# Kernel optimization log

Measured on AMD Instinct MI355X. Metric: run time of the kernel, lower is better.

Reference implementation:

```python
import jax, jax.numpy as jnp
import numpy as np

NUM_INST = 32
EPS = 1e-5


def _conv(x, w, b, stride=1, pad=0):
    y = jax.lax.conv_general_dilated(
        x, w, (stride, stride), ((pad, pad), (pad, pad)),
        dimension_numbers=('NCHW', 'OIHW', 'NCHW'))
    return y + b[None, :, None, None]


def _deconv(x, w, b):
    # torch ConvTranspose2d(k=3, s=2, p=1, output_padding=1); w is (Cin, Cout, 3, 3)
    wf = jnp.flip(w, (2, 3)).transpose(1, 0, 2, 3)  # -> OIHW
    y = jax.lax.conv_general_dilated(
        x, wf, (1, 1), ((1, 2), (1, 2)), lhs_dilation=(2, 2),
        dimension_numbers=('NCHW', 'OIHW', 'NCHW'))
    return y + b[None, :, None, None]


def _inorm(x):
    m = x.mean((2, 3), keepdims=True)
    v = x.var((2, 3), keepdims=True)  # biased, matches InstanceNorm2d
    return (x - m) * jax.lax.rsqrt(v + EPS)


def _rpad(x, p=3):
    return jnp.pad(x, ((0, 0), (0, 0), (p, p), (p, p)), mode='reflect')


def _backbone(input, w0, b0, w1, b1, w2, b2, w3, b3, w4, b4,
              w5, b5, w6, b6, w7, b7, w8, b8, w9, b9):
    x = jax.nn.relu(_inorm(_conv(_rpad(input), w0, b0)))          # [B,16,H,W]
    x = jax.nn.relu(_inorm(_conv(x, w1, b1, stride=2, pad=1)))    # [B,32,H/2,..]
    x = jax.nn.relu(_inorm(_conv(x, w2, b2, stride=2, pad=1)))    # [B,64,H/4,..]
    x = jax.nn.relu(_inorm(_conv(x, w3, b3, stride=2, pad=1)))    # [B,128,H/8,..]
    x = jax.nn.relu(_inorm(_conv(x, w4, b4, stride=2, pad=1)))    # [B,256,H/16,..]
    x = jax.nn.relu(_inorm(_deconv(x, w5, b5)))                   # [B,128,H/8,..]
    x = jax.nn.relu(_inorm(_deconv(x, w6, b6)))                   # [B,64,H/4,..]
    x = jax.nn.relu(_inorm(_deconv(x, w7, b7)))                   # [B,32,H/2,..]
    x = jax.nn.relu(_inorm(_deconv(x, w8, b8)))                   # [B,16,H,W]
    return jnp.tanh(_conv(_rpad(x), w9, b9))                      # [B,Cout,H,W]


def _segment_mean(outputs, inst):
    # outputs [B,C,H,W]; inst [B,1,H,W] int labels shared across the batch.
    B, C, H, W = outputs.shape
    seg = inst.reshape(-1)                                # [B*H*W]
    feats = outputs.transpose(0, 2, 3, 1).reshape(-1, C)  # [B*H*W, C]
    sums = jax.ops.segment_sum(feats, seg, num_segments=NUM_INST)
    counts = jax.ops.segment_sum(jnp.ones((feats.shape[0],), feats.dtype), seg,
                                 num_segments=NUM_INST)
    means = sums / jnp.maximum(counts, 1.0)[:, None]      # [NUM_INST, C]
    out = means[seg].reshape(B, H, W, C).transpose(0, 3, 1, 2)
    return out


def setup_inputs() -> dict:
    key = jax.random.key(0)
    ks = jax.random.split(key, 16)
    B, Cin, Cout, H, W = 4, 3, 3, 512, 512
    inp = {
        'input': jax.random.normal(ks[0], (B, Cin, H, W), jnp.float32),
        'inst': jax.random.randint(ks[1], (B, 1, H, W), 0, NUM_INST, jnp.int32),
    }
    std = 0.02
    # conv weights OIHW; deconv weights torch-style (Cin, Cout, kH, kW)
    shapes = [
        ('w0', (16, Cin, 7, 7)), ('w1', (32, 16, 3, 3)), ('w2', (64, 32, 3, 3)),
        ('w3', (128, 64, 3, 3)), ('w4', (256, 128, 3, 3)),
        ('w5', (256, 128, 3, 3)), ('w6', (128, 64, 3, 3)),
        ('w7', (64, 32, 3, 3)), ('w8', (32, 16, 3, 3)), ('w9', (Cout, 16, 7, 7)),
    ]
    bias_dims = [16, 32, 64, 128, 256, 128, 64, 32, 16, Cout]
    for i, (name, shp) in enumerate(shapes):
        inp[name] = std * jax.random.normal(ks[2 + i], shp, jnp.float32)
        inp['b%d' % i] = jnp.zeros((bias_dims[i],), jnp.float32)
    return inp


def reference(input, inst, w0, b0, w1, b1, w2, b2, w3, b3, w4, b4,
              w5, b5, w6, b6, w7, b7, w8, b8, w9, b9):
    outputs = _backbone(input, w0, b0, w1, b1, w2, b2, w3, b3, w4, b4,
                        w5, b5, w6, b6, w7, b7, w8, b8, w9, b9)
    return _segment_mean(outputs, inst)
```

## Files before the change

### kernel.cpp

```cpp
#include <hip/hip_runtime.h>
#include <math.h>

#define EPS_F 1e-5f

typedef __attribute__((ext_vector_type(8))) short short8;
typedef __attribute__((ext_vector_type(4))) float f32x4;
typedef __attribute__((ext_vector_type(8))) unsigned short ushort8;
typedef __attribute__((ext_vector_type(4))) unsigned short ushort4v;
typedef __attribute__((ext_vector_type(4))) int int4v;

__device__ __forceinline__ int reflect512(int v) {
    v = v < 0 ? -v : v;
    return v >= 512 ? 1022 - v : v;
}

__device__ __forceinline__ int xcd_swz(int L, int n) {
    return (L & 7) * (n >> 3) + (L >> 3);
}

__device__ __forceinline__ ushort f2bf(float f) {
    union { float f; unsigned u; } v; v.f = f;
    unsigned r = v.u + 0x7FFFu + ((v.u >> 16) & 1u);
    return (ushort)(r >> 16);
}
__device__ __forceinline__ float bf2f(ushort u) {
    union { unsigned u; float f; } v; v.u = (unsigned)u << 16;
    return v.f;
}

__device__ __forceinline__ unsigned cvt_pk_bf16(float lo, float hi) {
    unsigned r;
    asm("v_cvt_pk_bf16_f32 %0, %1, %2" : "=v"(r) : "v"(lo), "v"(hi));
    return r;
}

__device__ __forceinline__ float fast_tanh(float x) {
    float cx = fminf(fmaxf(x, -9.f), 9.f);
    float e  = __builtin_amdgcn_exp2f(cx * 2.8853900817779268f);
    return (e - 1.f) * __builtin_amdgcn_rcpf(e + 1.f);
}

template<int CIN, int COUT, bool DEC>
__device__ __forceinline__ void wp_mid(
    const float* __restrict__ w, ushort* __restrict__ dst, int i)
{
    constexpr int CIP = ((CIN + 31) / 32) * 32;
    int ci = i % CIP;
    int oc = (i / CIP) % COUT;
    int t  = i / (CIP * COUT);
    float x = 0.f;
    if (ci < CIN)
        x = DEC ? w[((size_t)ci * COUT + oc) * 9 + t]
                : w[((size_t)oc * CIN + ci) * 9 + t];
    dst[i] = f2bf(x);
}

__device__ __forceinline__ void wp_l1(
    const float* __restrict__ w, ushort* __restrict__ dst, int i)
{
    int k  = i & 31;
    int oc = (i >> 5) & 31;
    int c  = i >> 10;
    int tapsel = k >> 4, ci = k & 15;
    int t = 2 * c + tapsel;
    float x = (t < 9) ? w[((size_t)oc * 16 + ci) * 9 + t] : 0.f;
    dst[i] = f2bf(x);
}

template<bool L9>
__device__ __forceinline__ void wp_7(
    const float* __restrict__ w, ushort* __restrict__ dst, int i)
{
    int j   = i & 7;
    int oc  = (i >> 3) & 15;
    int kqe = (i >> 7) & 3;
    int cn  = i >> 9;
    float x = 0.f;
    if (L9) {
        int k = kqe * 8 + j;
        int tapsel = k >> 4, ci = k & 15;
        int ty = cn >> 2, q = cn & 3;
        int tx = 2 * q + tapsel;
        if (tx < 7 && oc < 3 && ty < 7)
            x = w[((size_t)oc * 16 + ci) * 49 + ty * 7 + tx];
    } else {
        int k = kqe * 8 + j;
        int dx = k >> 2, ci = k & 3;
        if (dx < 7 && ci < 3)
            x = w[((size_t)oc * 3 + ci) * 49 + cn * 7 + dx];
    }
    dst[i] = f2bf(x);
}

struct WprepArgs {
    const float* w[10];
    ushort* d[10];
};

__global__ __launch_bounds__(256) void wprep_all(WprepArgs a)
{
    int bi = blockIdx.x;
    int t  = threadIdx.x;
    if      (bi < 20)   wp_l1(a.w[1], a.d[1], (bi        ) * 256 + t);
    else if (bi < 92)   wp_mid<32,  64,  false>(a.w[2], a.d[2], (bi - 20   ) * 256 + t);
    else if (bi < 380)  wp_mid<64,  128, false>(a.w[3], a.d[3], (bi - 92   ) * 256 + t);
    else if (bi < 1532) wp_mid<128, 256, false>(a.w[4], a.d[4], (bi - 380  ) * 256 + t);
    else if (bi < 2684) wp_mid<256, 128, true >(a.w[5], a.d[5], (bi - 1532 ) * 256 + t);
    else if (bi < 2972) wp_mid<128, 64,  true >(a.w[6], a.d[6], (bi - 2684 ) * 256 + t);
    else if (bi < 3044) wp_mid<64,  32,  true >(a.w[7], a.d[7], (bi - 2972 ) * 256 + t);
    else if (bi < 3062) wp_mid<32,  16,  true >(a.w[8], a.d[8], (bi - 3044 ) * 256 + t);
    else if (bi < 3076) wp_7<false>(a.w[0], a.d[0], (bi - 3062) * 256 + t);
    else                wp_7<true >(a.w[9], a.d[9], (bi - 3076) * 256 + t);
}

template<int CIN, int COUT, int WIN, int MODE, int NWN, int MSUB, int RT, int CT>
__global__ __launch_bounds__(256) void mfconv(
    const ushort* __restrict__ in, const ushort* __restrict__ wbf,
    const float* __restrict__ bias, ushort* __restrict__ out,
    const float* __restrict__ stats_in, float invHWin,
    float* __restrict__ stats_out)
{
    constexpr int HWIN = WIN * WIN;
    constexpr int WOUT = (MODE == 0) ? (WIN / 2) : (WIN * 2);
    constexpr int HWOUT = WOUT * WOUT;
    constexpr int NMG = 4 / NWN;
    constexpr int NOC = NWN * 16;
    constexpr int M = NMG * MSUB * 16;
    static_assert(M == RT * CT, "tile mismatch");
    constexpr int SPAN = (MODE == 0) ? WOUT : WIN;
    constexpr int XC = SPAN / CT, YC = SPAN / RT;
    constexpr int NG = COUT / NOC;
    constexpr int NR = (MODE == 0) ? (2 * RT + 1) : (RT + 1);
    constexpr int NCO = (MODE == 0) ? (2 * CT + 1) : (CT + 1);
    constexpr int NPIX = NR * NCO;
    constexpr int CIP = ((CIN + 31) / 32) * 32;
    constexpr int NQ = (MODE == 0) ? 1 : 4;
    constexpr int LPW = 36;
    constexpr int NPOUT = (MODE == 0 ? 1 : 4) * M;
    constexpr int NOCP = NOC + 8;

    constexpr int TDY[9] = {1,1,1,0,0,0,0,0,0};
    constexpr int TDX[9] = {1,0,0,1,0,0,1,0,0};
    constexpr int TQ [9] = {3,2,3,1,0,1,3,2,3};

    extern __shared__ ushort sa[];
    __shared__ float mrall[CIP][2];
    __shared__ float sred[4][16][2];

    const int tid = threadIdx.x;
    const int lane = tid & 63, wv = tid >> 6;
    const int ln = lane & 15, kq = lane >> 4;
    const int wn = wv % NWN, wm = wv / NWN;
    const int grp = tid & 3;

    int bi = xcd_swz(blockIdx.x, gridDim.x);
    const int xc = bi % XC; bi /= XC;
    const int yc = bi % YC; bi /= YC;
    const int g  = bi % NG;
    const int b  = bi / NG;

    const int ocg = g * NOC + wn * 16 + ln;
    const float b0 = bias[ocg];
    f32x4 acc[NQ][MSUB];
    #pragma unroll
    for (int q = 0; q < NQ; q++)
        #pragma unroll
        for (int s = 0; s < MSUB; s++)
            acc[q][s] = (f32x4){b0, b0, b0, b0};

    for (int e = tid; e < CIP; e += 256) {
        float m = 0.f, r = 0.f;
        if (e < CIN) {
            int c = b * CIN + e;
            float s1 = stats_in[2 * c], s2 = stats_in[2 * c + 1];
            m = s1 * invHWin;
            r = rsqrtf(fmaf(s2, invHWin, -m * m) + EPS_F);
        }
        mrall[e][0] = m; mrall[e][1] = r;
    }

    const ushort* inb = in + (size_t)b * HWIN * CIN;

    for (int c0 = 0; c0 < CIP; c0 += 32) {
        __syncthreads();
        const int ch0 = c0 + 8 * grp;
        float m8[8], r8[8];
        #pragma unroll
        for (int j = 0; j < 8; j++) { m8[j] = mrall[ch0 + j][0]; r8[j] = mrall[ch0 + j][1]; }
        for (int pix = tid >> 2; pix < NPIX; pix += 64) {
            int pr = pix / NCO, pc = pix - pr * NCO;
            int gy, gx;
            if (MODE == 0) { gy = 2 * (yc * RT) - 1 + pr; gx = 2 * (xc * CT) - 1 + pc; }
            else           { gy = yc * RT + pr;           gx = xc * CT + pc; }
            ushort8 pk;
            #pragma unroll
            for (int j = 0; j < 8; j++) pk[j] = 0;
            if ((unsigned)gy < (unsigned)WIN && (unsigned)gx < (unsigned)WIN && ch0 < CIN) {
                ushort8 raw = *(const ushort8*)(inb + (size_t)(gy * WIN + gx) * CIN + ch0);
                #pragma unroll
                for (int j = 0; j < 8; j++) {
                    float x = bf2f(raw[j]);
                    pk[j] = f2bf(fmaxf((x - m8[j]) * r8[j], 0.f));
                }
            }
            *(ushort8*)&sa[pix * LPW + grp * 8] = pk;
        }
        __syncthreads();
        #pragma unroll
        for (int t = 0; t < 9; t++) {
            short8 bfr = *(const short8*)&wbf[((size_t)t * COUT + ocg) * CIP + c0 + kq * 8];
            #pragma unroll
            for (int s = 0; s < MSUB; s++) {
                const int mb = wm * MSUB * 16 + s * 16;
                const int r = mb / CT, cb = mb % CT;
                int pix;
                if (MODE == 0) pix = (t / 3 + 2 * r) * NCO + 2 * (cb + ln) + t % 3;
                else           pix = (TDY[t] + r) * NCO + cb + ln + TDX[t];
                short8 afr = *(const short8*)&sa[pix * LPW + kq * 8];
                int qd = (MODE == 0) ? 0 : TQ[t];
                acc[qd][s] = __builtin_amdgcn_mfma_f32_16x16x32_bf16(afr, bfr, acc[qd][s], 0, 0, 0);
            }
        }
    }

    float s1 = 0.f, s2 = 0.f;
    #pragma unroll
    for (int q = 0; q < NQ; q++)
        #pragma unroll
        for (int s = 0; s < MSUB; s++)
            #pragma unroll
            for (int rg = 0; rg < 4; rg++) {
                float v = acc[q][s][rg];
                s1 += v; s2 = fmaf(v, v, s2);
            }
    s1 += __shfl_xor(s1, 16); s2 += __shfl_xor(s2, 16);
    s1 += __shfl_xor(s1, 32); s2 += __shfl_xor(s2, 32);
    if (lane < 16) { sred[wv][lane][0] = s1; sred[wv][lane][1] = s2; }

    __syncthreads();
    const int ocl = wn * 16 + ln;
    if (MODE == 0) {
        #pragma unroll
        for (int s = 0; s < MSUB; s++)
            #pragma unroll
            for (int rg = 0; rg < 4; rg++) {
                const int m = wm * MSUB * 16 + s * 16 + kq * 4 + rg;
                sa[m * NOCP + ocl] = f2bf(acc[0][s][rg]);
            }
    } else {
        #pragma unroll
        for (int q = 0; q < 4; q++) {
            const int dy = q >> 1, dx = q & 1;
            #pragma unroll
            for (int s = 0; s < MSUB; s++)
                #pragma unroll
                for (int rg = 0; rg < 4; rg++) {
                    const int m = wm * MSUB * 16 + s * 16 + kq * 4 + rg;
                    const int r = m / CT, c = m % CT;
                    const int lp = (2 * r + dy) * (2 * CT) + 2 * c + dx;
                    sa[lp * NOCP + ocl] = f2bf(acc[q][s][rg]);
                }
        }
    }
    __syncthreads();

    ushort* ob = out + (size_t)b * HWOUT * COUT + g * NOC;
    for (int e = tid; e < (NPOUT * NOC) / 8; e += 256) {
        int u = e * 8;
        int lp = u / NOC, co = u % NOC;
        int gp;
        if (MODE == 0) {
            int r = lp / CT, c = lp % CT;
            gp = (yc * RT + r) * WOUT + xc * CT + c;
        } else {
            int r2 = lp / (2 * CT), x2 = lp % (2 * CT);
            gp = (2 * (yc * RT) + r2) * WOUT + 2 * (xc * CT) + x2;
        }
        *(ushort8*)&ob[(size_t)gp * COUT + co] = *(const ushort8*)&sa[lp * NOCP + co];
    }

    if (tid < NOC) {
        int wnn = tid >> 4, oc = tid & 15;
        float t1 = 0.f, t2 = 0.f;
        #pragma unroll
        for (int k = 0; k < NMG; k++) {
            t1 += sred[wnn + k * NWN][oc][0];
            t2 += sred[wnn + k * NWN][oc][1];
        }
        int cix = b * COUT + g * NOC + wnn * 16 + oc;
        atomicAdd(&stats_out[2 * cix],     t1);
        atomicAdd(&stats_out[2 * cix + 1], t2);
    }
}

__global__ __launch_bounds__(256) void mfconv_l1(
    const ushort* __restrict__ in, const ushort* __restrict__ wbf,
    const float* __restrict__ bias, ushort* __restrict__ out,
    const float* __restrict__ stats_in, float invHWin,
    float* __restrict__ stats_out)
{
    constexpr int WIN = 512, HWIN = WIN * WIN;
    constexpr int WOUT = 256, HWOUT = WOUT * WOUT;
    constexpr int COUT = 32, RT = 4, CT = 32;
    constexpr int NCO = 65, NPIX = 585;
    constexpr int NOCP = 40;

    extern __shared__ ushort sa[];
    __shared__ float mrall[16][2];
    __shared__ float sred[4][16][2];

    const int tid = threadIdx.x;
    const int lane = tid & 63, wv = tid >> 6;
    const int ln = lane & 15, kq = lane >> 4;
    const int wn = wv & 1, wm = wv >> 1;

    int bi = xcd_swz(blockIdx.x, gridDim.x);
    const int xc = bi & 7;
    const int yc = (bi >> 3) & 63;
    const int b  = bi >> 9;

    const int ocg = wn * 16 + ln;
    const float b0 = bias[ocg];
    f32x4 acc[4];
    #pragma unroll
    for (int s = 0; s < 4; s++) acc[s] = (f32x4){b0, b0, b0, b0};

    if (tid < 16) {
        int c = b * 16 + tid;
        float s1 = stats_in[2 * c], s2 = stats_in[2 * c + 1];
        float m = s1 * invHWin;
        mrall[tid][0] = m;
        mrall[tid][1] = rsqrtf(fmaf(s2, invHWin, -m * m) + EPS_F);
    }

    const int grp = tid & 1, p0 = tid >> 1;
    const ushort* inb = in + (size_t)b * HWIN * 16 + grp * 8;
    ushort8 rw[5];
    bool ok[5];
    #pragma unroll
    for (int i = 0; i < 5; i++) {
        int pix = p0 + i * 128;
        int pr = pix / NCO, pc = pix - pr * NCO;
        int gy = 2 * (yc * RT) - 1 + pr;
        int gx = 2 * (xc * CT) - 1 + pc;
        ok[i] = (pix < NPIX) && ((unsigned)gy < (unsigned)WIN)
                             && ((unsigned)gx < (unsigned)WIN);
        if (ok[i])
            rw[i] = *(const ushort8*)(inb + (size_t)(gy * WIN + gx) * 16);
    }
    __syncthreads();

    float m8[8], r8[8];
    #pragma unroll
    for (int j = 0; j < 8; j++) {
        m8[j] = mrall[grp * 8 + j][0];
        r8[j] = mrall[grp * 8 + j][1];
    }
    #pragma unroll
    for (int i = 0; i < 5; i++) {
        int pix = p0 + i * 128;
        if (pix < NPIX) {
            ushort8 pk;
            #pragma unroll
            for (int j = 0; j < 8; j++) pk[j] = 0;
            if (ok[i]) {
                #pragma unroll
                for (int j = 0; j < 8; j++) {
                    float x = bf2f(rw[i][j]);
                    pk[j] = f2bf(fmaxf((x - m8[j]) * r8[j], 0.f));
                }
            }
            int ep = (pix * 16 + grp * 8) ^ (((pix >> 2) & 1) << 3);
            *(ushort8*)&sa[ep] = pk;
        }
    }
    __syncthreads();

    const int tp = kq >> 1, off8 = (kq & 1) * 8;
    #pragma unroll
    for (int c = 0; c < 5; c++) {
        short8 bfr = *(const short8*)&wbf[(size_t)(c * COUT + ocg) * 32 + kq * 8];
        int t = 2 * c + tp; t = t > 8 ? 8 : t;
        const int ty = t / 3, tx = t - 3 * ty;
        #pragma unroll
        for (int s = 0; s < 4; s++) {
            const int mb = wm * 64 + s * 16;
            const int r = mb >> 5, cb = mb & 31;
            int px = (ty + 2 * r) * NCO + 2 * (cb + ln) + tx;
            int ep = (px * 16 + off8) ^ (((px >> 2) & 1) << 3);
            short8 afr = *(const short8*)&sa[ep];
            acc[s] = __builtin_amdgcn_mfma_f32_16x16x32_bf16(afr, bfr, acc[s], 0, 0, 0);
        }
    }

    float s1 = 0.f, s2 = 0.f;
    #pragma unroll
    for (int s = 0; s < 4; s++)
        #pragma unroll
        for (int rg = 0; rg < 4; rg++) {
            float v = acc[s][rg];
            s1 += v; s2 = fmaf(v, v, s2);
        }
    s1 += __shfl_xor(s1, 16); s2 += __shfl_xor(s2, 16);
    s1 += __shfl_xor(s1, 32); s2 += __shfl_xor(s2, 32);
    if (lane < 16) { sred[wv][lane][0] = s1; sred[wv][lane][1] = s2; }

    __syncthreads();
    const int ocl = wn * 16 + ln;
    #pragma unroll
    for (int s = 0; s < 4; s++)
        #pragma unroll
        for (int rg = 0; rg < 4; rg++) {
            const int m = wm * 64 + s * 16 + kq * 4 + rg;
            sa[m * NOCP + ocl] = f2bf(acc[s][rg]);
        }
    __syncthreads();
    ushort* ob = out + (size_t)b * HWOUT * COUT;
    for (int e = tid; e < 512; e += 256) {
        int u = e * 8;
        int lp = u >> 5, co = u & 31;
        int r = lp >> 5, c = lp & 31;
        int gp = (yc * RT + r) * WOUT + xc * CT + c;
        *(ushort8*)&ob[(size_t)gp * COUT + co] = *(const ushort8*)&sa[lp * NOCP + co];
    }
    if (tid < 32) {
        int wnn = tid >> 4, oc = tid & 15;
        float t1 = 0.f, t2 = 0.f;
        #pragma unroll
        for (int k = 0; k < 2; k++) {
            t1 += sred[wnn + k * 2][oc][0];
            t2 += sred[wnn + k * 2][oc][1];
        }
        int cix = b * COUT + wnn * 16 + oc;
        atomicAdd(&stats_out[2 * cix],     t1);
        atomicAdd(&stats_out[2 * cix + 1], t2);
    }
}

template<bool BFIN, bool SEG>
__global__ __launch_bounds__(256, 4) void conv7x(
    const float* __restrict__ inf, const ushort* __restrict__ inb16,
    const ushort* __restrict__ wpk, const float* __restrict__ bias,
    ushort* __restrict__ out,
    const float* __restrict__ stats_in, float invHWin,
    float* __restrict__ stats_out,
    const int* __restrict__ inst, float* __restrict__ segacc)
{
    constexpr int W = 512, HW = 512 * 512;
    constexpr int TCOL = BFIN ? 32 : 64;
    constexpr int HCOL = TCOL + 6;
    constexpr int NPIXH = 14 * HCOL;
    constexpr int STR = BFIN ? 16 : 4;
    constexpr int SASZ = BFIN ? (532 * 16 + 32) : 12288;
    constexpr int XCN = 512 / TCOL;
    constexpr int NS = BFIN ? 4 : 8;

    __shared__ ushort sa[SASZ];
    __shared__ float mr[16][2];
    __shared__ float segl[SEG ? 128 : 1];
    __shared__ float sred[4][16][2];

    const int tid = threadIdx.x;
    const int lane = tid & 63, wv = tid >> 6;
    const int ln = lane & 15, kq = lane >> 4;

    int bi = xcd_swz(blockIdx.x, gridDim.x);
    const int xc = bi % XCN;
    const int yr = (bi / XCN) & 63;
    const int b  = bi / (XCN * 64);
    const int y0 = yr * 8, x0 = xc * TCOL;

    if constexpr (SEG) { if (tid < 128) segl[tid] = 0.f; }
    if constexpr (BFIN) {
        if (tid < 16) {
            int c = b * 16 + tid;
            float s1 = stats_in[2 * c], s2 = stats_in[2 * c + 1];
            float m = s1 * invHWin;
            mr[tid][0] = m;
            mr[tid][1] = rsqrtf(fmaf(s2, invHWin, -m * m) + EPS_F);
        }
        if (tid >= 32 && tid < 64) sa[532 * 16 + (tid - 32)] = 0;
        __syncthreads();
        const int h = tid & 1;
        float r8[8], nm8[8];
        #pragma unroll
        for (int j = 0; j < 8; j++) {
            r8[j]  = mr[8 * h + j][1];
            nm8[j] = -mr[8 * h + j][0] * r8[j];
        }
        const ushort* inb = inb16 + (size_t)b * HW * 16 + 8 * h;
        for (int pix = tid >> 1; pix < NPIXH; pix += 128) {
            int pr = pix / HCOL, pc = pix - pr * HCOL;
            int gy = reflect512(y0 - 3 + pr);
            int gx = reflect512(x0 - 3 + pc);
            ushort8 raw = *(const ushort8*)(inb + (size_t)(gy * W + gx) * 16);
            union { ushort8 us; unsigned u[4]; } P;
            #pragma unroll
            for (int q2 = 0; q2 < 4; q2++) {
                float lo = fmaxf(fmaf(bf2f(raw[2 * q2]),     r8[2 * q2],     nm8[2 * q2]),     0.f);
                float hi = fmaxf(fmaf(bf2f(raw[2 * q2 + 1]), r8[2 * q2 + 1], nm8[2 * q2 + 1]), 0.f);
                P.u[q2] = cvt_pk_bf16(lo, hi);
            }
            *(ushort8*)&sa[pix * STR + 8 * h] = P.us;
        }
    } else {
        const float* p0 = inf + (size_t)b * 3 * HW;
        for (int pix = tid; pix < NPIXH; pix += 256) {
            int pr = pix / HCOL, pc = pix - pr * HCOL;
            int gy = reflect512(y0 - 3 + pr);
            int gx = reflect512(x0 - 3 + pc);
            const float* p = p0 + gy * W + gx;
            ushort4v pk;
            pk[0] = f2bf(p[0]); pk[1] = f2bf(p[HW]);
            pk[2] = f2bf(p[2 * (size_t)HW]); pk[3] = 0;
            *(ushort4v*)&sa[pix * 4] = pk;
        }
        if (tid < 16) sa[980 * 4 + tid] = 0;
    }
    __syncthreads();

    const float b0 = (ln < (BFIN ? 3 : 16)) ? bias[ln] : 0.f;
    f32x4 acc[NS];
    #pragma unroll
    for (int s = 0; s < NS; s++) acc[s] = (f32x4){b0, b0, b0, b0};

    if constexpr (BFIN) {
        const int wr = wv >> 1, wc = wv & 1;
        const int abase = ((wr * 4) * HCOL + wc * 16 + ln + (kq >> 1)) * STR + (kq & 1) * 8;
        const ushort* wp9 = wpk + ((size_t)kq * 16 + ln) * 8;
        #pragma unroll
        for (int q = 0; q < 4; q++) {
            short8 bw[7];
            #pragma unroll
            for (int ty = 0; ty < 7; ty++)
                bw[ty] = *(const short8*)(wp9 + (size_t)(ty * 4 + q) * 512);
            #pragma unroll
            for (int rr = 0; rr < 10; rr++) {
                short8 afr = *(const short8*)&sa[abase + q * (2 * STR) + rr * (HCOL * STR)];
                #pragma unroll
                for (int ty = 0; ty < 7; ty++) {
                    const int s = rr - ty;
                    if (s >= 0 && s < 4)
                        acc[s] = __builtin_amdgcn_mfma_f32_16x16x32_bf16(afr, bw[ty], acc[s], 0, 0, 0);
                }
            }
        }
    } else {
        const int c0 = wv * 16;
        const int abase = (c0 + ln + 2 * kq) * 4;
        const ushort* wp0 = wpk + ((size_t)kq * 16 + ln) * 8;
        short8 bw[7];
        #pragma unroll
        for (int ty = 0; ty < 7; ty++)
            bw[ty] = *(const short8*)(wp0 + (size_t)ty * 512);
        #pragma unroll
        for (int R = 0; R < 14; R++) {
            short8 afr = *(const short8*)&sa[abase + R * (HCOL * 4)];
            #pragma unroll
            for (int ty = 0; ty < 7; ty++) {
                const int s = R - ty;
                if (s >= 0 && s < 8)
                    acc[s] = __builtin_amdgcn_mfma_f32_16x16x32_bf16(afr, bw[ty], acc[s], 0, 0, 0);
            }
        }
    }

    if constexpr (SEG) {
        const int wr = wv >> 1, wc = wv & 1;
        float* sf = (float*)sa;
        __syncthreads();
        if (ln < 3) {
            #pragma unroll
            for (int s = 0; s < 4; s++)
                #pragma unroll
                for (int rg = 0; rg < 4; rg++) {
                    int m = (wr * 4 + s) * 32 + wc * 16 + kq * 4 + rg;
                    sf[m * 5 + ln] = acc[s][rg];
                }
        }
        __syncthreads();
        const int* ib = inst + ((size_t)b << 18);
        {
            int p2 = tid;
            int r = p2 >> 5, c = p2 & 31;
            int lab = ib[(y0 + r) * W + x0 + c] & 31;
            atomicAdd(&segl[lab * 4 + 0], fast_tanh(sf[p2 * 5 + 0]));
            atomicAdd(&segl[lab * 4 + 1], fast_tanh(sf[p2 * 5 + 1]));
            atomicAdd(&segl[lab * 4 + 2], fast_tanh(sf[p2 * 5 + 2]));
            atomicAdd(&segl[lab * 4 + 3], 1.f);
        }
        __syncthreads();
        if (tid < 128) {
            float v = segl[tid];
            if (v != 0.f)
                atomicAdd(&segacc[(blockIdx.x & 7) * 128 + tid], v);
        }
    } else {
        float s1 = 0.f, s2 = 0.f;
        #pragma unroll
        for (int s = 0; s < NS; s++)
            #pragma unroll
            for (int rg = 0; rg < 4; rg++) {
                float v = acc[s][rg];
                s1 += v; s2 = fmaf(v, v, s2);
            }
        s1 += __shfl_xor(s1, 16); s2 += __shfl_xor(s2, 16);
        s1 += __shfl_xor(s1, 32); s2 += __shfl_xor(s2, 32);
        if (lane < 16) { sred[wv][lane][0] = s1; sred[wv][lane][1] = s2; }

        __syncthreads();
        #pragma unroll
        for (int s = 0; s < 8; s++)
            #pragma unroll
            for (int rg = 0; rg < 4; rg++) {
                int m = s * 64 + wv * 16 + kq * 4 + rg;
                sa[m * 24 + ln] = f2bf(acc[s][rg]);
            }
        __syncthreads();
        ushort* ob = out + (size_t)b * HW * 16;
        for (int e = tid; e < 1024; e += 256) {
            int u = e * 8;
            int lp = u >> 4, co = u & 15;
            int gp = (y0 + (lp >> 6)) * W + x0 + (lp & 63);
            *(ushort8*)&ob[(size_t)gp * 16 + co] = *(const ushort8*)&sa[lp * 24 + co];
        }
        if (tid < 16) {
            float t1 = 0.f, t2 = 0.f;
            #pragma unroll
            for (int k = 0; k < 4; k++) { t1 += sred[k][tid][0]; t2 += sred[k][tid][1]; }
            int cix = b * 16 + tid;
            atomicAdd(&stats_out[2 * cix],     t1);
            atomicAdd(&stats_out[2 * cix + 1], t2);
        }
    }
}

#define HW9 262144
__global__ void seg_final(const float* __restrict__ acc, float* __restrict__ means)
{
    int i = threadIdx.x;
    if (i < 96) {
        int s = i / 3, c = i - s * 3;
        float num = 0.f, den = 0.f;
        #pragma unroll
        for (int k = 0; k < 8; k++) {
            num += acc[k * 128 + s * 4 + c];
            den += acc[k * 128 + s * 4 + 3];
        }
        means[i] = num / fmaxf(den, 1.f);
    }
}

__global__ __launch_bounds__(256) void seg_scatter(
    const int* __restrict__ inst, const float* __restrict__ means,
    float* __restrict__ out)
{
    int p4 = blockIdx.x * 256 + threadIdx.x;
    int b  = p4 >> 16;
    int r4 = (p4 & 65535) * 4;
    const int4v labs = *(const int4v*)(inst + ((size_t)b << 18) + r4);
    float* ob = out + (size_t)b * 3 * HW9 + r4;
    f32x4 o0, o1, o2;
    #pragma unroll
    for (int j = 0; j < 4; j++) {
        int l3 = (labs[j] & 31) * 3;
        o0[j] = means[l3]; o1[j] = means[l3 + 1]; o2[j] = means[l3 + 2];
    }
    *(f32x4*)(ob)           = o0;
    *(f32x4*)(ob + HW9)     = o1;
    *(f32x4*)(ob + 2 * HW9) = o2;
}

extern "C" void kernel_launch(void* const* d_in, const int* in_sizes, int n_in,
                              void* d_out, int out_size, void* d_ws, size_t ws_size,
                              hipStream_t stream)
{
    const float* x_in = (const float*)d_in[0];
    const int*   inst = (const int*)d_in[1];
    const float* W_[10];
    const float* Bs[10];
    for (int i = 0; i < 10; i++) {
        W_[i] = (const float*)d_in[2 + 2 * i];
        Bs[i] = (const float*)d_in[3 + 2 * i];
    }
    float* out = (float*)d_out;

    ushort* Ab  = (ushort*)d_ws;
    ushort* Bb2 = Ab + (size_t)16777216;
    float*  st  = (float*)(Bb2 + (size_t)8388608);
    const int coff[9] = {0, 128, 384, 896, 1920, 3968, 4992, 5504, 5760};
    float* s_[9];
    for (int i = 0; i < 9; i++) s_[i] = st + coff[i];
    float* segacc = st + 5888;
    float* means  = st + 6912;
    ushort* wb = (ushort*)(st + 8192);
    const size_t OW1 = 0, OW2 = 9216, OW3 = 27648, OW4 = 101376,
                 OW5 = 396288, OW6 = 691200, OW7 = 764928, OW8 = 783360;
    ushort* wb0 = wb + 790000;
    ushort* wb9 = wb0 + 6656;

    hipMemsetAsync(st, 0, 6912 * sizeof(float), stream);

    WprepArgs wa;
    for (int i = 0; i < 10; i++) wa.w[i] = W_[i];
    wa.d[0] = wb0;
    wa.d[1] = wb + OW1; wa.d[2] = wb + OW2; wa.d[3] = wb + OW3; wa.d[4] = wb + OW4;
    wa.d[5] = wb + OW5; wa.d[6] = wb + OW6; wa.d[7] = wb + OW7; wa.d[8] = wb + OW8;
    wa.d[9] = wb9;
    wprep_all<<<dim3(3132), dim3(256), 0, stream>>>(wa);

    conv7x<false, false><<<dim3(2048), dim3(256), 0, stream>>>(
        x_in, nullptr, wb0, Bs[0], Ab, nullptr, 0.f, s_[0], nullptr, nullptr);

    mfconv_l1<<<dim3(2048), dim3(256), 18720, stream>>>(
        Ab, wb + OW1, Bs[1], Bb2, s_[0], 1.f / 262144.f, s_[1]);

    mfconv<32, 64, 256, 0, 2, 4, 4, 32><<<dim3(1024), dim3(256), 42120, stream>>>(
        Bb2, wb + OW2, Bs[2], Ab, s_[1], 1.f / 65536.f, s_[2]);

    mfconv<64, 128, 128, 0, 2, 4, 4, 32><<<dim3(512), dim3(256), 42120, stream>>>(
        Ab, wb + OW3, Bs[3], Bb2, s_[2], 1.f / 16384.f, s_[3]);

    mfconv<128, 256, 64, 0, 2, 2, 2, 32><<<dim3(512), dim3(256), 23400, stream>>>(
        Bb2, wb + OW4, Bs[4], Ab, s_[3], 1.f / 4096.f, s_[4]);

    mfconv<256, 128, 32, 1, 1, 1, 2, 32><<<dim3(512), dim3(256), 12288, stream>>>(
        Ab, wb + OW5, Bs[5], Bb2, s_[4], 1.f / 1024.f, s_[5]);

    mfconv<128, 64, 64, 1, 2, 2, 2, 32><<<dim3(512), dim3(256), 20480, stream>>>(
        Bb2, wb + OW6, Bs[6], Ab, s_[5], 1.f / 4096.f, s_[6]);

    mfconv<64, 32, 128, 1, 2, 2, 2, 32><<<dim3(1024), dim3(256), 20480, stream>>>(
        Ab, wb + OW7, Bs[7], Bb2, s_[6], 1.f / 16384.f, s_[7]);

    mfconv<32, 16, 256, 1, 1, 2, 2, 64><<<dim3(2048), dim3(256), 24576, stream>>>(
        Bb2, wb + OW8, Bs[8], Ab, s_[7], 1.f / 65536.f, s_[8]);

    conv7x<true, true><<<dim3(4096), dim3(256), 0, stream>>>(
        nullptr, Ab, wb9, Bs[9], nullptr, s_[8], 1.f / 262144.f, nullptr, inst, segacc);

    seg_final<<<dim3(1), dim3(96), 0, stream>>>(segacc, means);
    seg_scatter<<<dim3(1024), dim3(256), 0, stream>>>(inst, means, out);
}
```

Measured before the change: 419.7 us.

## Split final 7x7 conv into persistent double-buffered kernel processing four tiles per block

The final 7x7 conv with fused segment accumulation moves into its own kernel. Each block now handles four consecutive 32-column tiles, using double-buffered shared-memory staging so the global loads for the next tile overlap the MFMA work on the current one. Instance labels are also prefetched, and the per-block segment partials are flushed once after all four tiles rather than once per tile. The launch shrinks from 4096 to 1024 blocks, which cuts per-block setup and global atomics but doubles LDS use and may lower occupancy.

```diff
diff --git a/kernel.cpp b/kernel.cpp
--- a/kernel.cpp
+++ b/kernel.cpp
@@ -437,27 +437,18 @@
     }
 }
 
-template<bool BFIN, bool SEG>
+template<bool BFIN>
 __global__ __launch_bounds__(256, 4) void conv7x(
-    const float* __restrict__ inf, const ushort* __restrict__ inb16,
+    const float* __restrict__ inf,
     const ushort* __restrict__ wpk, const float* __restrict__ bias,
-    ushort* __restrict__ out,
-    const float* __restrict__ stats_in, float invHWin,
-    float* __restrict__ stats_out,
-    const int* __restrict__ inst, float* __restrict__ segacc)
+    ushort* __restrict__ out, float* __restrict__ stats_out)
 {
     constexpr int W = 512, HW = 512 * 512;
-    constexpr int TCOL = BFIN ? 32 : 64;
-    constexpr int HCOL = TCOL + 6;
-    constexpr int NPIXH = 14 * HCOL;
-    constexpr int STR = BFIN ? 16 : 4;
-    constexpr int SASZ = BFIN ? (532 * 16 + 32) : 12288;
-    constexpr int XCN = 512 / TCOL;
-    constexpr int NS = BFIN ? 4 : 8;
+    constexpr int HCOL = 70;
+    constexpr int NPIXH = 980;
+    constexpr int SASZ = 12288;
 
     __shared__ ushort sa[SASZ];
-    __shared__ float mr[16][2];
-    __shared__ float segl[SEG ? 128 : 1];
     __shared__ float sred[4][16][2];
 
     const int tid = threadIdx.x;
@@ -465,45 +456,12 @@
     const int ln = lane & 15, kq = lane >> 4;
 
     int bi = xcd_swz(blockIdx.x, gridDim.x);
-    const int xc = bi % XCN;
-    const int yr = (bi / XCN) & 63;
-    const int b  = bi / (XCN * 64);
-    const int y0 = yr * 8, x0 = xc * TCOL;
-
-    if constexpr (SEG) { if (tid < 128) segl[tid] = 0.f; }
-    if constexpr (BFIN) {
-        if (tid < 16) {
-            int c = b * 16 + tid;
-            float s1 = stats_in[2 * c], s2 = stats_in[2 * c + 1];
-            float m = s1 * invHWin;
-            mr[tid][0] = m;
-            mr[tid][1] = rsqrtf(fmaf(s2, invHWin, -m * m) + EPS_F);
-        }
-        if (tid >= 32 && tid < 64) sa[532 * 16 + (tid - 32)] = 0;
-        __syncthreads();
-        const int h = tid & 1;
-        float r8[8], nm8[8];
-        #pragma unroll
-        for (int j = 0; j < 8; j++) {
-            r8[j]  = mr[8 * h + j][1];
-            nm8[j] = -mr[8 * h + j][0] * r8[j];
-        }
-        const ushort* inb = inb16 + (size_t)b * HW * 16 + 8 * h;
-        for (int pix = tid >> 1; pix < NPIXH; pix += 128) {
-            int pr = pix / HCOL, pc = pix - pr * HCOL;
-            int gy = reflect512(y0 - 3 + pr);
-            int gx = reflect512(x0 - 3 + pc);
-            ushort8 raw = *(const ushort8*)(inb + (size_t)(gy * W + gx) * 16);
-            union { ushort8 us; unsigned u[4]; } P;
-            #pragma unroll
-            for (int q2 = 0; q2 < 4; q2++) {
-                float lo = fmaxf(fmaf(bf2f(raw[2 * q2]),     r8[2 * q2],     nm8[2 * q2]),     0.f);
-                float hi = fmaxf(fmaf(bf2f(raw[2 * q2 + 1]), r8[2 * q2 + 1], nm8[2 * q2 + 1]), 0.f);
-                P.u[q2] = cvt_pk_bf16(lo, hi);
-            }
-            *(ushort8*)&sa[pix * STR + 8 * h] = P.us;
-        }
-    } else {
+    const int xc = bi & 7;
+    const int yr = (bi >> 3) & 63;
+    const int b  = bi >> 9;
+    const int y0 = yr * 8, x0 = xc * 64;
+
+    {
         const float* p0 = inf + (size_t)b * 3 * HW;
         for (int pix = tid; pix < NPIXH; pix += 256) {
             int pr = pix / HCOL, pc = pix - pr * HCOL;
@@ -519,15 +477,166 @@
     }
     __syncthreads();
 
-    const float b0 = (ln < (BFIN ? 3 : 16)) ? bias[ln] : 0.f;
-    f32x4 acc[NS];
-    #pragma unroll
-    for (int s = 0; s < NS; s++) acc[s] = (f32x4){b0, b0, b0, b0};
-
-    if constexpr (BFIN) {
-        const int wr = wv >> 1, wc = wv & 1;
-        const int abase = ((wr * 4) * HCOL + wc * 16 + ln + (kq >> 1)) * STR + (kq & 1) * 8;
-        const ushort* wp9 = wpk + ((size_t)kq * 16 + ln) * 8;
+    const float b0 = bias[ln];
+    f32x4 acc[8];
+    #pragma unroll
+    for (int s = 0; s < 8; s++) acc[s] = (f32x4){b0, b0, b0, b0};
+
+    {
+        const int c0 = wv * 16;
+        const int abase = (c0 + ln + 2 * kq) * 4;
+        const ushort* wp0 = wpk + ((size_t)kq * 16 + ln) * 8;
+        short8 bw[7];
+        #pragma unroll
+        for (int ty = 0; ty < 7; ty++)
+            bw[ty] = *(const short8*)(wp0 + (size_t)ty * 512);
+        #pragma unroll
+        for (int R = 0; R < 14; R++) {
+            short8 afr = *(const short8*)&sa[abase + R * (HCOL * 4)];
+            #pragma unroll
+            for (int ty = 0; ty < 7; ty++) {
+                const int s = R - ty;
+                if (s >= 0 && s < 8)
+                    acc[s] = __builtin_amdgcn_mfma_f32_16x16x32_bf16(afr, bw[ty], acc[s], 0, 0, 0);
+            }
+        }
+    }
+
+    float s1 = 0.f, s2 = 0.f;
+    #pragma unroll
+    for (int s = 0; s < 8; s++)
+        #pragma unroll
+        for (int rg = 0; rg < 4; rg++) {
+            float v = acc[s][rg];
+            s1 += v; s2 = fmaf(v, v, s2);
+        }
+    s1 += __shfl_xor(s1, 16); s2 += __shfl_xor(s2, 16);
+    s1 += __shfl_xor(s1, 32); s2 += __shfl_xor(s2, 32);
+    if (lane < 16) { sred[wv][lane][0] = s1; sred[wv][lane][1] = s2; }
+
+    __syncthreads();
+    #pragma unroll
+    for (int s = 0; s < 8; s++)
+        #pragma unroll
+        for (int rg = 0; rg < 4; rg++) {
+            int m = s * 64 + wv * 16 + kq * 4 + rg;
+            sa[m * 24 + ln] = f2bf(acc[s][rg]);
+        }
+    __syncthreads();
+    ushort* ob = out + (size_t)b * HW * 16;
+    for (int e = tid; e < 1024; e += 256) {
+        int u = e * 8;
+        int lp = u >> 4, co = u & 15;
+        int gp = (y0 + (lp >> 6)) * W + x0 + (lp & 63);
+        *(ushort8*)&ob[(size_t)gp * 16 + co] = *(const ushort8*)&sa[lp * 24 + co];
+    }
+    if (tid < 16) {
+        float t1 = 0.f, t2 = 0.f;
+        #pragma unroll
+        for (int k = 0; k < 4; k++) { t1 += sred[k][tid][0]; t2 += sred[k][tid][1]; }
+        int cix = b * 16 + tid;
+        atomicAdd(&stats_out[2 * cix],     t1);
+        atomicAdd(&stats_out[2 * cix + 1], t2);
+    }
+}
+
+__global__ __launch_bounds__(256, 4) void conv7x_l9p(
+    const ushort* __restrict__ inb16, const ushort* __restrict__ wpk,
+    const float* __restrict__ bias, const float* __restrict__ stats_in,
+    float invHWin, const int* __restrict__ inst, float* __restrict__ segacc)
+{
+    constexpr int W = 512, HW = 512 * 512;
+    constexpr int HCOL = 38, STR = 16;
+    constexpr int SA1 = 8544;
+
+    __shared__ ushort sa[2][SA1];
+    __shared__ float sf[1280];
+    __shared__ float mr[16][2];
+    __shared__ float segl[128];
+
+    const int tid = threadIdx.x;
+    const int lane = tid & 63, wv = tid >> 6;
+    const int ln = lane & 15, kq = lane >> 4;
+
+    const int L  = (blockIdx.x & 7) * 128 + (blockIdx.x >> 3);
+    const int t0 = L * 4;
+    const int b  = t0 >> 10;
+    const int yr = (t0 >> 4) & 63;
+    const int xcb = t0 & 15;
+    const int y0 = yr * 8;
+
+    const int h = tid & 1;
+    const ushort* inbb = inb16 + (size_t)b * HW * 16 + 8 * h;
+    const int* ib = inst + ((size_t)b << 18);
+
+    ushort8 rw[5];
+
+#define L9_ISSUE(X0) do {                                                   \
+    _Pragma("unroll")                                                       \
+    for (int i2 = 0; i2 < 5; i2++) {                                        \
+        int pix = (tid >> 1) + i2 * 128;                                    \
+        if (pix < 532) {                                                    \
+            int pr = pix / HCOL, pc = pix - pr * HCOL;                      \
+            int gy = reflect512(y0 - 3 + pr);                               \
+            int gx = reflect512((X0) - 3 + pc);                             \
+            rw[i2] = *(const ushort8*)(inbb + (size_t)(gy * W + gx) * 16);  \
+        } } } while (0)
+
+#define L9_WRITE(BUF) do {                                                  \
+    _Pragma("unroll")                                                       \
+    for (int i2 = 0; i2 < 5; i2++) {                                        \
+        int pix = (tid >> 1) + i2 * 128;                                    \
+        if (pix < 532) {                                                    \
+            union { ushort8 us; unsigned u[4]; } P;                         \
+            _Pragma("unroll")                                               \
+            for (int q2 = 0; q2 < 4; q2++) {                                \
+                float lo = fmaxf(fmaf(bf2f(rw[i2][2*q2]),   r8[2*q2],   nm8[2*q2]),   0.f); \
+                float hi = fmaxf(fmaf(bf2f(rw[i2][2*q2+1]), r8[2*q2+1], nm8[2*q2+1]), 0.f); \
+                P.u[q2] = cvt_pk_bf16(lo, hi);                              \
+            }                                                               \
+            *(ushort8*)&sa[BUF][pix * STR + 8 * h] = P.us;                  \
+        } } } while (0)
+
+    L9_ISSUE(xcb * 32);
+    if (tid < 16) {
+        int c = b * 16 + tid;
+        float s1 = stats_in[2 * c], s2 = stats_in[2 * c + 1];
+        float m = s1 * invHWin;
+        mr[tid][0] = m;
+        mr[tid][1] = rsqrtf(fmaf(s2, invHWin, -m * m) + EPS_F);
+    }
+    if (tid < 128) segl[tid] = 0.f;
+    if (tid >= 128 && tid < 160) {
+        sa[0][8512 + (tid - 128)] = 0;
+        sa[1][8512 + (tid - 128)] = 0;
+    }
+    __syncthreads();
+
+    float r8[8], nm8[8];
+    #pragma unroll
+    for (int j = 0; j < 8; j++) {
+        r8[j]  = mr[8 * h + j][1];
+        nm8[j] = -mr[8 * h + j][0] * r8[j];
+    }
+    L9_WRITE(0);
+    int lab_next = ib[(y0 + (tid >> 5)) * W + xcb * 32 + (tid & 31)] & 31;
+    __syncthreads();
+
+    const int wr = wv >> 1, wc = wv & 1;
+    const int abase = ((wr * 4) * HCOL + wc * 16 + ln + (kq >> 1)) * STR + (kq & 1) * 8;
+    const ushort* wp9 = wpk + ((size_t)kq * 16 + ln) * 8;
+    const float b0 = (ln < 3) ? bias[ln] : 0.f;
+
+    for (int it = 0; it < 4; ++it) {
+        const int cur = it & 1;
+        const int mylab = lab_next;
+        if (it < 3) {
+            L9_ISSUE((xcb + it + 1) * 32);
+            lab_next = ib[(y0 + (tid >> 5)) * W + (xcb + it + 1) * 32 + (tid & 31)] & 31;
+        }
+        f32x4 acc[4];
+        #pragma unroll
+        for (int s = 0; s < 4; s++) acc[s] = (f32x4){b0, b0, b0, b0};
         #pragma unroll
         for (int q = 0; q < 4; q++) {
             short8 bw[7];
@@ -536,7 +645,7 @@
                 bw[ty] = *(const short8*)(wp9 + (size_t)(ty * 4 + q) * 512);
             #pragma unroll
             for (int rr = 0; rr < 10; rr++) {
-                short8 afr = *(const short8*)&sa[abase + q * (2 * STR) + rr * (HCOL * STR)];
+                short8 afr = *(const short8*)&sa[cur][abase + q * (2 * STR) + rr * (HCOL * STR)];
                 #pragma unroll
                 for (int ty = 0; ty < 7; ty++) {
                     const int s = rr - ty;
@@ -545,30 +654,7 @@
                 }
             }
         }
-    } else {
-        const int c0 = wv * 16;
-        const int abase = (c0 + ln + 2 * kq) * 4;
-        const ushort* wp0 = wpk + ((size_t)kq * 16 + ln) * 8;
-        short8 bw[7];
-        #pragma unroll
-        for (int ty = 0; ty < 7; ty++)
-            bw[ty] = *(const short8*)(wp0 + (size_t)ty * 512);
-        #pragma unroll
-        for (int R = 0; R < 14; R++) {
-            short8 afr = *(const short8*)&sa[abase + R * (HCOL * 4)];
-            #pragma unroll
-            for (int ty = 0; ty < 7; ty++) {
-                const int s = R - ty;
-                if (s >= 0 && s < 8)
-                    acc[s] = __builtin_amdgcn_mfma_f32_16x16x32_bf16(afr, bw[ty], acc[s], 0, 0, 0);
-            }
-        }
-    }
-
-    if constexpr (SEG) {
-        const int wr = wv >> 1, wc = wv & 1;
-        float* sf = (float*)sa;
-        __syncthreads();
+        if (it < 3) L9_WRITE(cur ^ 1);
         if (ln < 3) {
             #pragma unroll
             for (int s = 0; s < 4; s++)
@@ -579,60 +665,20 @@
                 }
         }
         __syncthreads();
-        const int* ib = inst + ((size_t)b << 18);
-        {
-            int p2 = tid;
-            int r = p2 >> 5, c = p2 & 31;
-            int lab = ib[(y0 + r) * W + x0 + c] & 31;
-            atomicAdd(&segl[lab * 4 + 0], fast_tanh(sf[p2 * 5 + 0]));
-            atomicAdd(&segl[lab * 4 + 1], fast_tanh(sf[p2 * 5 + 1]));
-            atomicAdd(&segl[lab * 4 + 2], fast_tanh(sf[p2 * 5 + 2]));
-            atomicAdd(&segl[lab * 4 + 3], 1.f);
-        }
+        atomicAdd(&segl[mylab * 4 + 0], fast_tanh(sf[tid * 5 + 0]));
+        atomicAdd(&segl[mylab * 4 + 1], fast_tanh(sf[tid * 5 + 1]));
+        atomicAdd(&segl[mylab * 4 + 2], fast_tanh(sf[tid * 5 + 2]));
+        atomicAdd(&segl[mylab * 4 + 3], 1.f);
         __syncthreads();
-        if (tid < 128) {
-            float v = segl[tid];
-            if (v != 0.f)
-                atomicAdd(&segacc[(blockIdx.x & 7) * 128 + tid], v);
-        }
-    } else {
-        float s1 = 0.f, s2 = 0.f;
-        #pragma unroll
-        for (int s = 0; s < NS; s++)
-            #pragma unroll
-            for (int rg = 0; rg < 4; rg++) {
-                float v = acc[s][rg];
-                s1 += v; s2 = fmaf(v, v, s2);
-            }
-        s1 += __shfl_xor(s1, 16); s2 += __shfl_xor(s2, 16);
-        s1 += __shfl_xor(s1, 32); s2 += __shfl_xor(s2, 32);
-        if (lane < 16) { sred[wv][lane][0] = s1; sred[wv][lane][1] = s2; }
-
-        __syncthreads();
-        #pragma unroll
-        for (int s = 0; s < 8; s++)
-            #pragma unroll
-            for (int rg = 0; rg < 4; rg++) {
-                int m = s * 64 + wv * 16 + kq * 4 + rg;
-                sa[m * 24 + ln] = f2bf(acc[s][rg]);
-            }
-        __syncthreads();
-        ushort* ob = out + (size_t)b * HW * 16;
-        for (int e = tid; e < 1024; e += 256) {
-            int u = e * 8;
-            int lp = u >> 4, co = u & 15;
-            int gp = (y0 + (lp >> 6)) * W + x0 + (lp & 63);
-            *(ushort8*)&ob[(size_t)gp * 16 + co] = *(const ushort8*)&sa[lp * 24 + co];
-        }
-        if (tid < 16) {
-            float t1 = 0.f, t2 = 0.f;
-            #pragma unroll
-            for (int k = 0; k < 4; k++) { t1 += sred[k][tid][0]; t2 += sred[k][tid][1]; }
-            int cix = b * 16 + tid;
-            atomicAdd(&stats_out[2 * cix],     t1);
-            atomicAdd(&stats_out[2 * cix + 1], t2);
-        }
-    }
+    }
+
+    if (tid < 128) {
+        float v = segl[tid];
+        if (v != 0.f)
+            atomicAdd(&segacc[(blockIdx.x & 7) * 128 + tid], v);
+    }
+#undef L9_ISSUE
+#undef L9_WRITE
 }
 
 #define HW9 262144
@@ -709,8 +755,8 @@
     wa.d[9] = wb9;
     wprep_all<<<dim3(3132), dim3(256), 0, stream>>>(wa);
 
-    conv7x<false, false><<<dim3(2048), dim3(256), 0, stream>>>(
-        x_in, nullptr, wb0, Bs[0], Ab, nullptr, 0.f, s_[0], nullptr, nullptr);
+    conv7x<false><<<dim3(2048), dim3(256), 0, stream>>>(
+        x_in, wb0, Bs[0], Ab, s_[0]);
 
     mfconv_l1<<<dim3(2048), dim3(256), 18720, stream>>>(
         Ab, wb + OW1, Bs[1], Bb2, s_[0], 1.f / 262144.f, s_[1]);
@@ -736,8 +782,8 @@
     mfconv<32, 16, 256, 1, 1, 2, 2, 64><<<dim3(2048), dim3(256), 24576, stream>>>(
         Bb2, wb + OW8, Bs[8], Ab, s_[7], 1.f / 65536.f, s_[8]);
 
-    conv7x<true, true><<<dim3(4096), dim3(256), 0, stream>>>(
-        nullptr, Ab, wb9, Bs[9], nullptr, s_[8], 1.f / 262144.f, nullptr, inst, segacc);
+    conv7x_l9p<<<dim3(1024), dim3(256), 0, stream>>>(
+        Ab, wb9, Bs[9], s_[8], 1.f / 262144.f, inst, segacc);
 
     seg_final<<<dim3(1), dim3(96), 0, stream>>>(segacc, means);
     seg_scatter<<<dim3(1024), dim3(256), 0, stream>>>(inst, means, out);
```

New measurement: 489.6 us. +16.7%, slower.
